# Kernel optimization log

Measured on AMD Instinct MI355X. Metric: run time of the kernel, lower is better.

The kernel has to match this reference:

```python
import jax, jax.numpy as jnp
import numpy as np

EPS = 1e-5  # pyg LayerNorm default eps


def _graph_ln(x):
    # pyg.nn.norm.LayerNorm(affine=False), default mode='graph', batch=None:
    # normalizes over ALL elements of the tensor (x - x.mean()) / x.std(unbiased=False)
    m = x.mean()
    v = jnp.mean((x - m) ** 2)
    return (x - m) * jax.lax.rsqrt(v + EPS)


def _cheb_conv(x, row, col, w, W, b):
    # ChebConv, normalization='sym', lambda_max=2 => scaled Laplacian
    # L_hat = L - I = -D^{-1/2} A D^{-1/2} (self-loops removed, weighted)
    # x: [B,N,C_in], row/col: [E], w: [E], W: [K,C_in,C_out], b: [C_out]
    N = x.shape[1]
    w = jnp.where(row == col, 0.0, w)  # remove_self_loops
    deg = jnp.zeros((N,), x.dtype).at[row].add(w)
    dinv = jnp.where(deg > 0, jax.lax.rsqrt(jnp.maximum(deg, 1e-12)), 0.0)
    norm = -(dinv[row] * w * dinv[col])  # [E]

    def prop(t):  # out[i] += norm_e * t[j] for edge (j=row -> i=col)
        msg = norm[None, :, None] * t[:, row, :]  # [B,E,C]
        return jnp.zeros_like(t).at[:, col, :].add(msg)

    Tx0 = x
    out = jnp.einsum('bnc,cd->bnd', Tx0, W[0])
    Tx1 = prop(x)
    out = out + jnp.einsum('bnc,cd->bnd', Tx1, W[1])
    for k in range(2, W.shape[0]):
        Tx2 = 2.0 * prop(Tx1) - Tx0
        out = out + jnp.einsum('bnc,cd->bnd', Tx2, W[k])
        Tx0, Tx1 = Tx1, Tx2
    return out + b


def setup_inputs() -> dict:
    key = jax.random.key(0)
    ks = jax.random.split(key, 8)
    B, N, C, E, L, K = 8, 2048, 256, 32768, 3, 3
    node_feature = jax.random.normal(ks[0], (B, N, C), dtype=jnp.float32)
    edge_index = jax.random.randint(ks[1], (L, 2, E), 0, N)
    edge_weight = jax.random.uniform(ks[2], (L, E), dtype=jnp.float32)
    s = 1.0 / np.sqrt(C)
    cheb_w = jax.random.normal(ks[3], (L, K, C, C), dtype=jnp.float32) * s
    cheb_b = jnp.zeros((L, C), dtype=jnp.float32)
    mlp_w = jax.random.normal(ks[4], (L, C, C), dtype=jnp.float32) * s
    mlp_b = jax.random.normal(ks[5], (L, C), dtype=jnp.float32) * 0.01
    return {"node_feature": node_feature, "edge_weight": edge_weight,
            "cheb_w": cheb_w, "cheb_b": cheb_b, "mlp_w": mlp_w,
            "mlp_b": mlp_b, "edge_index": edge_index}


def reference(node_feature, edge_weight, cheb_w, cheb_b, mlp_w, mlp_b, edge_index):
    h = node_feature  # [B,N,C]
    L = cheb_w.shape[0]
    for l in range(L):
        h_res = h
        hn = _graph_ln(h)
        hc = _cheb_conv(hn, edge_index[l, 0], edge_index[l, 1],
                        edge_weight[l], cheb_w[l], cheb_b[l])
        h = hc + h_res
        h_res = h
        hn = _graph_ln(h)
        hm = jax.nn.gelu(jnp.einsum('bnc,cd->bnd', hn, mlp_w[l]) + mlp_b[l],
                         approximate=False)  # dropout is identity at inference
        h = hm + h_res
    return h.mean(axis=1)  # [B,C]
```

## Files before the change

kernel.cpp:

```cpp
#include <hip/hip_runtime.h>

#define BATCH   8
#define NNODE   2048
#define CH      256
#define NEDGE   32768
#define NLAYER  3
#define MROWS   (NNODE*BATCH)
#define KCAT    (3*CH)
#define NTOT    (MROWS*CH)

typedef _Float16 half8 __attribute__((ext_vector_type(8)));
typedef _Float16 half4 __attribute__((ext_vector_type(4)));
typedef float    f32x4 __attribute__((ext_vector_type(4)));

#define OFF_ACAT   ((size_t)0)
#define OFF_HF     ((size_t)25165824)
#define OFF_WT     ((size_t)33554432)
#define OFF_MT     ((size_t)34734080)
#define OFF_PARTA  ((size_t)35127296)
#define OFF_PARTB  ((size_t)35135488)
#define OFF_CS     ((size_t)35143680)
#define OFF_CSM    ((size_t)35152896)
#define OFF_DEG    ((size_t)35155968)
#define OFF_CNT    ((size_t)35180544)
#define OFF_ELIST  ((size_t)35205120)
#define OFF_R1     ((size_t)36777984)
#define OFF_R2     ((size_t)36802560)

#define NPART 512

__device__ __forceinline__ void async_lds16(const void* g, void* l) {
  __builtin_amdgcn_global_load_lds((const __attribute__((address_space(1))) void*)g,
                                   (__attribute__((address_space(3))) void*)l, 16, 0, 0);
}

__global__ __launch_bounds__(256) void k_init(const float* __restrict__ x,
                                              _Float16* __restrict__ Acat,
                                              float2* __restrict__ part,
                                              const float* __restrict__ cheb_w,
                                              const float* __restrict__ mlp_w,
                                              _Float16* __restrict__ Wt,
                                              _Float16* __restrict__ Mt,
                                              float* __restrict__ deg,
                                              unsigned int* __restrict__ count) {
  __shared__ float rs[512];
  __shared__ _Float16 lt[64][72];
  const int blk = blockIdx.x, t = threadIdx.x;
  if (blk < 512) {
    int tid = blk*256 + t;
    float s = 0.f, s2 = 0.f;
    for (int i = tid; i < NTOT/4; i += 512*256) {
      int c4 = i & 63, b = (i >> 6) & 7, n = i >> 9;
      float4 v = ((const float4*)x)[((b*NNODE + n) << 6) + c4];
      half4 o; o[0]=(_Float16)v.x; o[1]=(_Float16)v.y; o[2]=(_Float16)v.z; o[3]=(_Float16)v.w;
      *(half4*)&Acat[(size_t)(i >> 6)*KCAT + c4*4] = o;
      s  += v.x + v.y + v.z + v.w;
      s2 += v.x*v.x + v.y*v.y + v.z*v.z + v.w*v.w;
    }
    rs[t] = s; rs[256+t] = s2; __syncthreads();
    for (int o = 128; o > 0; o >>= 1) {
      if (t < o) { rs[t] += rs[t+o]; rs[256+t] += rs[256+t+o]; }
      __syncthreads();
    }
    if (t == 0) part[blk] = make_float2(rs[0], rs[256]);
  } else if (blk < 536) {
    int i = (blk - 512)*256 + t;
    if (i < NLAYER*NNODE) { deg[i] = 0.f; count[i] = 0u; }
  } else {
    const int tile = blk - 536;
    const int rr = t >> 4, c4 = t & 15;
    if (tile < 144) {
      const int l = tile / 48, rem = tile % 48;
      const int kk = rem / 16, q = rem % 16, ci = q >> 2, ni = q & 3;
      const float4* W  = (const float4*)cheb_w + ((size_t)((l*3 + kk)*CH + ci*64))*64 + ni*16;
      const float4* W2 = (const float4*)cheb_w + ((size_t)((l*3 + 2 )*CH + ci*64))*64 + ni*16;
      #pragma unroll
      for (int p = 0; p < 4; ++p) {
        const int r = p*16 + rr;
        float4 v = W[(size_t)r*64 + c4];
        if (kk == 0) {
          float4 v2 = W2[(size_t)r*64 + c4];
          v.x -= v2.x; v.y -= v2.y; v.z -= v2.z; v.w -= v2.w;
        } else if (kk == 2) {
          v.x *= 2.f; v.y *= 2.f; v.z *= 2.f; v.w *= 2.f;
        }
        lt[c4*4+0][r] = (_Float16)v.x; lt[c4*4+1][r] = (_Float16)v.y;
        lt[c4*4+2][r] = (_Float16)v.z; lt[c4*4+3][r] = (_Float16)v.w;
      }
      __syncthreads();
      const int nr = t >> 2, ch2 = t & 3;
      #pragma unroll
      for (int pp = 0; pp < 2; ++pp) {
        const int ch = ch2 + pp*4;
        half8 v = *(const half8*)&lt[nr][ch*8];
        *(half8*)&Wt[((size_t)(l*CH + ni*64 + nr))*KCAT + kk*256 + ci*64 + ch*8] = v;
      }
    } else {
      const int m = tile - 144;
      const int l = m / 16, q = m % 16, ci = q >> 2, ni = q & 3;
      const float4* W = (const float4*)mlp_w + ((size_t)(l*CH + ci*64))*64 + ni*16;
      #pragma unroll
      for (int p = 0; p < 4; ++p) {
        const int r = p*16 + rr;
        float4 v = W[(size_t)r*64 + c4];
        lt[c4*4+0][r] = (_Float16)v.x; lt[c4*4+1][r] = (_Float16)v.y;
        lt[c4*4+2][r] = (_Float16)v.z; lt[c4*4+3][r] = (_Float16)v.w;
      }
      __syncthreads();
      const int nr = t >> 2, ch2 = t & 3;
      #pragma unroll
      for (int pp = 0; pp < 2; ++pp) {
        const int ch = ch2 + pp*4;
        half8 v = *(const half8*)&lt[nr][ch*8];
        *(half8*)&Mt[((size_t)(l*CH + ni*64 + nr))*CH + ci*64 + ch*8] = v;
      }
    }
  }
}

__global__ __launch_bounds__(256) void k_edge_scatter(const int* __restrict__ ei,
                                                      const float* __restrict__ ew,
                                                      float* deg, unsigned int* count,
                                                      unsigned int* elist,
                                                      const _Float16* __restrict__ Wt,
                                                      const _Float16* __restrict__ Mt,
                                                      float* __restrict__ cs,
                                                      float* __restrict__ csM,
                                                      float* __restrict__ out_zero) {
  const int blk = blockIdx.x, t = threadIdx.x;
  if (blk < 384) {
    int i = blk*256 + t;
    int l = i / NEDGE, e = i % NEDGE;
    const int* rows = ei + l*2*NEDGE;
    const int* cols = rows + NEDGE;
    int r = rows[e], c = cols[e];
    float w = (r == c) ? 0.f : ew[i];
    atomicAdd(&deg[l*NNODE + r], w);
    unsigned int slot = atomicAdd(&count[l*NNODE + c], 1u);
    if (slot < 64u) elist[(size_t)(l*NNODE + c)*64 + slot] = (unsigned int)e;
  } else if (blk < 393) {
    int idx = blk - 384, l = idx / 3, kk = idx % 3, n = t;
    const half8* row = (const half8*)&Wt[((size_t)(l*CH + n))*KCAT + kk*256];
    float s = 0.f;
    #pragma unroll 4
    for (int j = 0; j < 32; ++j) {
      half8 v = row[j];
      s += (float)v[0]+(float)v[1]+(float)v[2]+(float)v[3]
         + (float)v[4]+(float)v[5]+(float)v[6]+(float)v[7];
    }
    cs[(l*3 + kk)*CH + n] = s;
  } else if (blk < 396) {
    int l = blk - 393, n = t;
    const half8* row = (const half8*)&Mt[((size_t)(l*CH + n))*CH];
    float s = 0.f;
    #pragma unroll 4
    for (int j = 0; j < 32; ++j) {
      half8 v = row[j];
      s += (float)v[0]+(float)v[1]+(float)v[2]+(float)v[3]
         + (float)v[4]+(float)v[5]+(float)v[6]+(float)v[7];
    }
    csM[l*CH + n] = s;
  } else {
    for (int i = t; i < BATCH*CH; i += 256) out_zero[i] = 0.f;
  }
}

template<int SRC_OFF, int DST_OFF, int RMODE>
__global__ __launch_bounds__(256) void k_prop(_Float16* __restrict__ Acat,
                                              const int* __restrict__ rows,
                                              const float* __restrict__ ew_l,
                                              const float* __restrict__ deg_l,
                                              const unsigned int* __restrict__ count,
                                              const unsigned int* __restrict__ el,
                                              float* __restrict__ r1_l,
                                              float* __restrict__ r2_l) {
  const int blk = blockIdx.x, t = threadIdx.x;
  const int bp = blk & 3, dgrp = blk >> 2;
  const int w = t >> 6, lane = t & 63;
  const int dst = dgrp*4 + w;
  const int b = bp*2 + (lane >> 5), l32 = lane & 31;
  unsigned int c = count[dst]; if (c > 64u) c = 64u;
  const float dc = deg_l[dst];
  const float ic = dc > 0.f ? rsqrtf(fmaxf(dc, 1e-12f)) : 0.f;
  int srcv = 0; float nmv = 0.f;
  if (lane < (int)c) {
    unsigned int e = el[(size_t)dst*64 + lane];
    srcv = rows[e];
    float wv = (srcv == dst) ? 0.f : ew_l[e];
    float dr = deg_l[srcv];
    float ir = dr > 0.f ? rsqrtf(fmaxf(dr, 1e-12f)) : 0.f;
    nmv = -(ir * wv * ic);
  }
  if (RMODE && bp == 0) {
    float rv = nmv;
    if (RMODE == 2) rv = (lane < (int)c) ? nmv * r1_l[srcv] : 0.f;
    #pragma unroll
    for (int o = 32; o > 0; o >>= 1) rv += __shfl_xor(rv, o);
    if (lane == 0) { if (RMODE == 1) r1_l[dst] = rv; else r2_l[dst] = rv; }
  }
  float a0=0.f,a1=0.f,a2=0.f,a3=0.f,a4=0.f,a5=0.f,a6=0.f,a7=0.f;
  const _Float16* base = Acat + SRC_OFF + (size_t)b*KCAT + l32*8;
  #define PROP_STEP(i)                                                            \
    {                                                                             \
      int   src = __builtin_amdgcn_readlane(srcv, (i));                           \
      int   nbi = __builtin_amdgcn_readlane(__builtin_bit_cast(int, nmv), (i));   \
      float nm  = __builtin_bit_cast(float, nbi);                                 \
      half8 v = *(const half8*)&base[(size_t)src*8*KCAT];                         \
      a0 += nm*(float)v[0]; a1 += nm*(float)v[1];                                 \
      a2 += nm*(float)v[2]; a3 += nm*(float)v[3];                                 \
      a4 += nm*(float)v[4]; a5 += nm*(float)v[5];                                 \
      a6 += nm*(float)v[6]; a7 += nm*(float)v[7];                                 \
    }
  unsigned int i = 0;
  for (; i + 4 <= c; i += 4) { PROP_STEP(i) PROP_STEP(i+1) PROP_STEP(i+2) PROP_STEP(i+3) }
  for (; i < c; ++i) { PROP_STEP(i) }
  #undef PROP_STEP
  half8 o;
  o[0]=(_Float16)a0; o[1]=(_Float16)a1; o[2]=(_Float16)a2; o[3]=(_Float16)a3;
  o[4]=(_Float16)a4; o[5]=(_Float16)a5; o[6]=(_Float16)a6; o[7]=(_Float16)a7;
  *(half8*)&Acat[(size_t)(dst*8 + b)*KCAT + DST_OFF + l32*8] = o;
}

template<int KSTEPS, int DO_GELU>
__global__ __launch_bounds__(256) void k_gemm(const _Float16* __restrict__ A, int lda,
                                              const _Float16* __restrict__ Bt, int ldb,
                                              const float* __restrict__ bias,
                                              const float* __restrict__ cs,
                                              const float* __restrict__ r1,
                                              const float* __restrict__ r2,
                                              const float2* __restrict__ part_in,
                                              float2* __restrict__ part_out,
                                              const _Float16* __restrict__ R, int ldr,
                                              _Float16* __restrict__ O, int ldo) {
  __shared__ _Float16 Als[128*64];
  __shared__ _Float16 Bls[64*64];
  __shared__ float red[512];
  __shared__ float mv[2];
  const int bm = blockIdx.x, bn = blockIdx.y;
  const int t = threadIdx.x;
  const int w = t >> 6, lane = t & 63;
  const int quad = lane >> 4, l16 = lane & 15;
  const int rw = w & 1, cw = w >> 1;

  {
    float s = 0.f, s2 = 0.f;
    for (int i = t; i < NPART; i += 256) { float2 p = part_in[i]; s += p.x; s2 += p.y; }
    red[t] = s; red[256+t] = s2; __syncthreads();
    for (int o = 128; o > 0; o >>= 1) {
      if (t < o) { red[t] += red[t+o]; red[256+t] += red[256+t+o]; }
      __syncthreads();
    }
    if (t == 0) {
      float mean = red[0] * (1.f/(float)NTOT);
      float var  = red[256] * (1.f/(float)NTOT) - mean*mean;
      mv[0] = mean; mv[1] = rsqrtf(var + 1e-5f);
    }
    __syncthreads();
  }
  const float mean = mv[0], istd = mv[1];

  f32x4 acc[4][2];
  #pragma unroll
  for (int i = 0; i < 4; ++i)
    #pragma unroll
    for (int j = 0; j < 2; ++j) acc[i][j] = (f32x4){0.f,0.f,0.f,0.f};

  const int cA0 = t, cA1 = 256+t, cA2 = 512+t, cA3 = 768+t;
  const int rA0 = cA0>>3, sA0 = (cA0&7)^(rA0&7);
  const int rA1 = cA1>>3, sA1 = (cA1&7)^(rA1&7);
  const int rA2 = cA2>>3, sA2 = (cA2&7)^(rA2&7);
  const int rA3 = cA3>>3, sA3 = (cA3&7)^(rA3&7);
  const _Float16* ga0 = A + (size_t)(bm*128 + rA0)*lda + sA0*8;
  const _Float16* ga1 = A + (size_t)(bm*128 + rA1)*lda + sA1*8;
  const _Float16* ga2 = A + (size_t)(bm*128 + rA2)*lda + sA2*8;
  const _Float16* ga3 = A + (size_t)(bm*128 + rA3)*lda + sA3*8;
  const _Float16* gb0 = Bt + (size_t)(bn*64 + rA0)*ldb + sA0*8;
  const _Float16* gb1 = Bt + (size_t)(bn*64 + rA1)*ldb + sA1*8;
  _Float16* lA0 = &Als[w*512];
  _Float16* lA1 = &Als[2048 + w*512];
  _Float16* lA2 = &Als[4096 + w*512];
  _Float16* lA3 = &Als[6144 + w*512];
  _Float16* lB0 = &Bls[w*512];
  _Float16* lB1 = &Bls[2048 + w*512];

  for (int ks = 0; ks < KSTEPS; ++ks) {
    async_lds16(ga0, lA0); async_lds16(ga1, lA1);
    async_lds16(ga2, lA2); async_lds16(ga3, lA3);
    async_lds16(gb0, lB0); async_lds16(gb1, lB1);
    ga0 += 64; ga1 += 64; ga2 += 64; ga3 += 64; gb0 += 64; gb1 += 64;
    __syncthreads();
    #pragma unroll
    for (int kh = 0; kh < 2; ++kh) {
      const int q = kh*4 + quad;
      half8 bf[2];
      #pragma unroll
      for (int j = 0; j < 2; ++j) {
        const int rb = cw*32 + j*16 + l16;
        bf[j] = *(const half8*)&Bls[rb*64 + (q ^ (rb & 7))*8];
      }
      #pragma unroll
      for (int i = 0; i < 4; ++i) {
        const int ra = rw*64 + i*16 + l16;
        half8 af = *(const half8*)&Als[ra*64 + (q ^ (ra & 7))*8];
        acc[i][0] = __builtin_amdgcn_mfma_f32_16x16x32_f16(af, bf[0], acc[i][0], 0, 0, 0);
        acc[i][1] = __builtin_amdgcn_mfma_f32_16x16x32_f16(af, bf[1], acc[i][1], 0, 0, 0);
      }
    }
    __syncthreads();
  }

  float s = 0.f, s2 = 0.f;
  const int gm0 = bm*128 + rw*64, gn0 = bn*64 + cw*32;
  const float mi = -mean * istd;
  #pragma unroll
  for (int i = 0; i < 4; ++i) {
    #pragma unroll
    for (int j = 0; j < 2; ++j) {
      f32x4 a = acc[i][j];
      const int col = gn0 + j*16 + l16;
      const float bv = bias[col];
      const float c0v = cs[col];
      float c1v = 0.f, c2v = 0.f;
      if (!DO_GELU) { c1v = cs[256 + col]; c2v = cs[512 + col]; }
      #pragma unroll
      for (int r = 0; r < 4; ++r) {
        const int row = gm0 + i*16 + quad*4 + r;
        float v;
        if (DO_GELU) {
          v = istd*a[r] + mi*c0v + bv;
          v = 0.5f*v*(1.f + erff(v*0.70710678118654752f));
        } else {
          const int node = row >> 3;
          v = istd*a[r] + mi*(c0v + r1[node]*c1v + r2[node]*c2v) + bv;
        }
        float hv = (float)R[(size_t)row*ldr + col] + v;
        O[(size_t)row*ldo + col] = (_Float16)hv;
        s += hv; s2 += hv*hv;
      }
    }
  }
  red[t] = s; red[256+t] = s2; __syncthreads();
  for (int o = 128; o > 0; o >>= 1) {
    if (t < o) { red[t] += red[t+o]; red[256+t] += red[256+t+o]; }
    __syncthreads();
  }
  if (t == 0) part_out[blockIdx.y*gridDim.x + blockIdx.x] = make_float2(red[0], red[256]);
}

__global__ __launch_bounds__(256) void k_mean(const _Float16* __restrict__ Acat,
                                              float* __restrict__ out) {
  int b = blockIdx.x & 7, chunk = blockIdx.x >> 3;
  int c = threadIdx.x;
  float s = 0.f;
  for (int k = 0; k < 256; ++k) {
    int n = chunk*256 + k;
    s += (float)Acat[(size_t)(n*8 + b)*KCAT + c];
  }
  atomicAdd(&out[(b << 8) + c], s * (1.f/(float)NNODE));
}

extern "C" void kernel_launch(void* const* d_in, const int* in_sizes, int n_in,
                              void* d_out, int out_size, void* d_ws, size_t ws_size,
                              hipStream_t stream) {
  const float* x      = (const float*)d_in[0];
  const float* ew     = (const float*)d_in[1];
  const float* cheb_w = (const float*)d_in[2];
  const float* cheb_b = (const float*)d_in[3];
  const float* mlp_w  = (const float*)d_in[4];
  const float* mlp_b  = (const float*)d_in[5];
  const int*   ei     = (const int*)d_in[6];
  float* out = (float*)d_out;

  char* ws = (char*)d_ws;
  _Float16*     Acat  = (_Float16*)(ws + OFF_ACAT);
  _Float16*     Hf    = (_Float16*)(ws + OFF_HF);
  _Float16*     Wt    = (_Float16*)(ws + OFF_WT);
  _Float16*     Mt    = (_Float16*)(ws + OFF_MT);
  float2*       partA = (float2*)(ws + OFF_PARTA);
  float2*       partB = (float2*)(ws + OFF_PARTB);
  float*        cs    = (float*)(ws + OFF_CS);
  float*        csM   = (float*)(ws + OFF_CSM);
  float*        deg   = (float*)(ws + OFF_DEG);
  unsigned int* cnt   = (unsigned int*)(ws + OFF_CNT);
  unsigned int* elist = (unsigned int*)(ws + OFF_ELIST);
  float*        r1    = (float*)(ws + OFF_R1);
  float*        r2    = (float*)(ws + OFF_R2);

  k_init<<<728, 256, 0, stream>>>(x, Acat, partA, cheb_w, mlp_w, Wt, Mt, deg, cnt);
  k_edge_scatter<<<397, 256, 0, stream>>>(ei, ew, deg, cnt, elist, Wt, Mt, cs, csM, out);

  for (int l = 0; l < NLAYER; ++l) {
    const int* rows_l = ei + l*2*NEDGE;
    const float* ew_l = ew + l*NEDGE;
    const float* deg_l = deg + l*NNODE;
    const unsigned int* cnt_l = cnt + l*NNODE;
    const unsigned int* el_l  = elist + (size_t)l*NNODE*64;
    float* r1_l = r1 + l*NNODE;
    float* r2_l = r2 + l*NNODE;

    k_prop<0, 256, 1><<<2048, 256, 0, stream>>>(
        Acat, rows_l, ew_l, deg_l, cnt_l, el_l, r1_l, r2_l);
    k_prop<256, 512, 2><<<2048, 256, 0, stream>>>(
        Acat, rows_l, ew_l, deg_l, cnt_l, el_l, r1_l, r2_l);
    k_gemm<12, 0><<<dim3(128, 4), 256, 0, stream>>>(
        Acat, KCAT, Wt + (size_t)l*CH*KCAT, KCAT, cheb_b + l*CH,
        cs + l*3*CH, r1_l, r2_l, partA, partB,
        Acat, KCAT, Hf, CH);
    k_gemm<4, 1><<<dim3(128, 4), 256, 0, stream>>>(
        Hf, CH, Mt + (size_t)l*CH*CH, CH, mlp_b + l*CH,
        csM + l*CH, r1_l, r2_l, partB, partA,
        Hf, CH, Acat, KCAT);
  }

  k_mean<<<64, 256, 0, stream>>>(Acat, out);
}
```

Measured before the change: 274.8 us.

## Merge edge scatter into init kernel with LDS atomics; double GEMM K-tile

The separate edge-scatter kernel is folded into k_init. Each block now owns a 256-node slice of one layer, scans all edges and accumulates degree and in-edge counts with LDS atomics instead of global atomics. The column sums are computed directly from the fp32 weights, so they no longer depend on Wt/Mt being written first. The GEMM K-step tile is doubled from 64 to 128 with a 16-way XOR swizzle, which halves the number of barrier iterations but doubles shared memory per block and may lower occupancy. The redundant edge scans (each of 24 blocks reads every edge of its layer) add global read traffic, and the order of edge slots can differ from before.

```diff
diff --git a/kernel.cpp b/kernel.cpp
--- a/kernel.cpp
+++ b/kernel.cpp
@@ -39,14 +39,20 @@
                                               float2* __restrict__ part,
                                               const float* __restrict__ cheb_w,
                                               const float* __restrict__ mlp_w,
+                                              const float* __restrict__ ew,
+                                              const int* __restrict__ ei,
                                               _Float16* __restrict__ Wt,
                                               _Float16* __restrict__ Mt,
                                               float* __restrict__ deg,
-                                              unsigned int* __restrict__ count) {
-  __shared__ float rs[512];
-  __shared__ _Float16 lt[64][72];
+                                              unsigned int* __restrict__ cnt,
+                                              unsigned int* __restrict__ elist,
+                                              float* __restrict__ cs,
+                                              float* __restrict__ csM,
+                                              float* __restrict__ out_zero) {
+  __shared__ __align__(16) char smem[9216];
   const int blk = blockIdx.x, t = threadIdx.x;
   if (blk < 512) {
+    float* rs = (float*)smem;
     int tid = blk*256 + t;
     float s = 0.f, s2 = 0.f;
     for (int i = tid; i < NTOT/4; i += 512*256) {
@@ -64,9 +70,29 @@
     }
     if (t == 0) part[blk] = make_float2(rs[0], rs[256]);
   } else if (blk < 536) {
-    int i = (blk - 512)*256 + t;
-    if (i < NLAYER*NNODE) { deg[i] = 0.f; count[i] = 0u; }
-  } else {
+    unsigned int* cnt_lds = (unsigned int*)smem;
+    float*        deg_lds = (float*)(smem + 1024);
+    const int rel = blk - 512, l = rel >> 3, base = (rel & 7) << 8;
+    cnt_lds[t] = 0u; deg_lds[t] = 0.f; __syncthreads();
+    const int* rows = ei + l*2*NEDGE;
+    const int* cols = rows + NEDGE;
+    const float* ewl = ew + l*NEDGE;
+    for (int e = t; e < NEDGE; e += 256) {
+      int r = rows[e], c = cols[e];
+      float wv = (r == c) ? 0.f : ewl[e];
+      int cr = c - base;
+      if ((unsigned)cr < 256u) {
+        unsigned int slot = atomicAdd(&cnt_lds[cr], 1u);
+        if (slot < 64u) elist[((size_t)(l*NNODE + c) << 6) + slot] = (unsigned int)e;
+      }
+      int rr = r - base;
+      if ((unsigned)rr < 256u) atomicAdd(&deg_lds[rr], wv);
+    }
+    __syncthreads();
+    cnt[l*NNODE + base + t] = cnt_lds[t];
+    deg[l*NNODE + base + t] = deg_lds[t];
+  } else if (blk < 728) {
+    _Float16 (*lt)[72] = (_Float16(*)[72])smem;
     const int tile = blk - 536;
     const int rr = t >> 4, c4 = t & 15;
     if (tile < 144) {
@@ -115,51 +141,27 @@
         *(half8*)&Mt[((size_t)(l*CH + ni*64 + nr))*CH + ci*64 + ch*8] = v;
       }
     }
-  }
-}
-
-__global__ __launch_bounds__(256) void k_edge_scatter(const int* __restrict__ ei,
-                                                      const float* __restrict__ ew,
-                                                      float* deg, unsigned int* count,
-                                                      unsigned int* elist,
-                                                      const _Float16* __restrict__ Wt,
-                                                      const _Float16* __restrict__ Mt,
-                                                      float* __restrict__ cs,
-                                                      float* __restrict__ csM,
-                                                      float* __restrict__ out_zero) {
-  const int blk = blockIdx.x, t = threadIdx.x;
-  if (blk < 384) {
-    int i = blk*256 + t;
-    int l = i / NEDGE, e = i % NEDGE;
-    const int* rows = ei + l*2*NEDGE;
-    const int* cols = rows + NEDGE;
-    int r = rows[e], c = cols[e];
-    float w = (r == c) ? 0.f : ew[i];
-    atomicAdd(&deg[l*NNODE + r], w);
-    unsigned int slot = atomicAdd(&count[l*NNODE + c], 1u);
-    if (slot < 64u) elist[(size_t)(l*NNODE + c)*64 + slot] = (unsigned int)e;
-  } else if (blk < 393) {
-    int idx = blk - 384, l = idx / 3, kk = idx % 3, n = t;
-    const half8* row = (const half8*)&Wt[((size_t)(l*CH + n))*KCAT + kk*256];
-    float s = 0.f;
-    #pragma unroll 4
-    for (int j = 0; j < 32; ++j) {
-      half8 v = row[j];
-      s += (float)v[0]+(float)v[1]+(float)v[2]+(float)v[3]
-         + (float)v[4]+(float)v[5]+(float)v[6]+(float)v[7];
-    }
-    cs[(l*3 + kk)*CH + n] = s;
-  } else if (blk < 396) {
-    int l = blk - 393, n = t;
-    const half8* row = (const half8*)&Mt[((size_t)(l*CH + n))*CH];
-    float s = 0.f;
-    #pragma unroll 4
-    for (int j = 0; j < 32; ++j) {
-      half8 v = row[j];
-      s += (float)v[0]+(float)v[1]+(float)v[2]+(float)v[3]
-         + (float)v[4]+(float)v[5]+(float)v[6]+(float)v[7];
-    }
-    csM[l*CH + n] = s;
+  } else if (blk < 740) {
+    const int idx = blk - 728, n = t;
+    if (idx < 9) {
+      const int l = idx / 3, kk = idx % 3;
+      const float* W0 = cheb_w + (size_t)((l*3 + kk)*CH)*CH + n;
+      const float* W2 = cheb_w + (size_t)((l*3 + 2 )*CH)*CH + n;
+      float s = 0.f;
+      for (int cin = 0; cin < CH; ++cin) {
+        float wv = W0[(size_t)cin*CH];
+        if (kk == 0)      wv -= W2[(size_t)cin*CH];
+        else if (kk == 2) wv *= 2.f;
+        s += wv;
+      }
+      cs[(l*3 + kk)*CH + n] = s;
+    } else {
+      const int l = idx - 9;
+      const float* W = mlp_w + (size_t)l*CH*CH + n;
+      float s = 0.f;
+      for (int k2 = 0; k2 < CH; ++k2) s += W[(size_t)k2*CH];
+      csM[l*CH + n] = s;
+    }
   } else {
     for (int i = t; i < BATCH*CH; i += 256) out_zero[i] = 0.f;
   }
@@ -232,8 +234,8 @@
                                               float2* __restrict__ part_out,
                                               const _Float16* __restrict__ R, int ldr,
                                               _Float16* __restrict__ O, int ldo) {
-  __shared__ _Float16 Als[128*64];
-  __shared__ _Float16 Bls[64*64];
+  __shared__ _Float16 Als[128*128];
+  __shared__ _Float16 Bls[64*128];
   __shared__ float red[512];
   __shared__ float mv[2];
   const int bm = blockIdx.x, bn = blockIdx.y;
@@ -265,43 +267,42 @@
     #pragma unroll
     for (int j = 0; j < 2; ++j) acc[i][j] = (f32x4){0.f,0.f,0.f,0.f};
 
-  const int cA0 = t, cA1 = 256+t, cA2 = 512+t, cA3 = 768+t;
-  const int rA0 = cA0>>3, sA0 = (cA0&7)^(rA0&7);
-  const int rA1 = cA1>>3, sA1 = (cA1&7)^(rA1&7);
-  const int rA2 = cA2>>3, sA2 = (cA2&7)^(rA2&7);
-  const int rA3 = cA3>>3, sA3 = (cA3&7)^(rA3&7);
-  const _Float16* ga0 = A + (size_t)(bm*128 + rA0)*lda + sA0*8;
-  const _Float16* ga1 = A + (size_t)(bm*128 + rA1)*lda + sA1*8;
-  const _Float16* ga2 = A + (size_t)(bm*128 + rA2)*lda + sA2*8;
-  const _Float16* ga3 = A + (size_t)(bm*128 + rA3)*lda + sA3*8;
-  const _Float16* gb0 = Bt + (size_t)(bn*64 + rA0)*ldb + sA0*8;
-  const _Float16* gb1 = Bt + (size_t)(bn*64 + rA1)*ldb + sA1*8;
-  _Float16* lA0 = &Als[w*512];
-  _Float16* lA1 = &Als[2048 + w*512];
-  _Float16* lA2 = &Als[4096 + w*512];
-  _Float16* lA3 = &Als[6144 + w*512];
-  _Float16* lB0 = &Bls[w*512];
-  _Float16* lB1 = &Bls[2048 + w*512];
+  const _Float16* ga[8];
+  const _Float16* gb[4];
+  #pragma unroll
+  for (int j = 0; j < 8; ++j) {
+    const int c = j*256 + t, r = c >> 4, s = (c & 15) ^ (r & 15);
+    ga[j] = A + (size_t)(bm*128 + r)*lda + s*8;
+  }
+  #pragma unroll
+  for (int j = 0; j < 4; ++j) {
+    const int c = j*256 + t, r = c >> 4, s = (c & 15) ^ (r & 15);
+    gb[j] = Bt + (size_t)(bn*64 + r)*ldb + s*8;
+  }
 
   for (int ks = 0; ks < KSTEPS; ++ks) {
-    async_lds16(ga0, lA0); async_lds16(ga1, lA1);
-    async_lds16(ga2, lA2); async_lds16(ga3, lA3);
-    async_lds16(gb0, lB0); async_lds16(gb1, lB1);
-    ga0 += 64; ga1 += 64; ga2 += 64; ga3 += 64; gb0 += 64; gb1 += 64;
+    #pragma unroll
+    for (int j = 0; j < 8; ++j) async_lds16(ga[j], &Als[j*2048 + w*512]);
+    #pragma unroll
+    for (int j = 0; j < 4; ++j) async_lds16(gb[j], &Bls[j*2048 + w*512]);
+    #pragma unroll
+    for (int j = 0; j < 8; ++j) ga[j] += 128;
+    #pragma unroll
+    for (int j = 0; j < 4; ++j) gb[j] += 128;
     __syncthreads();
     #pragma unroll
-    for (int kh = 0; kh < 2; ++kh) {
+    for (int kh = 0; kh < 4; ++kh) {
       const int q = kh*4 + quad;
       half8 bf[2];
       #pragma unroll
       for (int j = 0; j < 2; ++j) {
         const int rb = cw*32 + j*16 + l16;
-        bf[j] = *(const half8*)&Bls[rb*64 + (q ^ (rb & 7))*8];
+        bf[j] = *(const half8*)&Bls[rb*128 + (q ^ (rb & 15))*8];
       }
       #pragma unroll
       for (int i = 0; i < 4; ++i) {
         const int ra = rw*64 + i*16 + l16;
-        half8 af = *(const half8*)&Als[ra*64 + (q ^ (ra & 7))*8];
+        half8 af = *(const half8*)&Als[ra*128 + (q ^ (ra & 15))*8];
         acc[i][0] = __builtin_amdgcn_mfma_f32_16x16x32_f16(af, bf[0], acc[i][0], 0, 0, 0);
         acc[i][1] = __builtin_amdgcn_mfma_f32_16x16x32_f16(af, bf[1], acc[i][1], 0, 0, 0);
       }
@@ -386,8 +387,8 @@
   float*        r1    = (float*)(ws + OFF_R1);
   float*        r2    = (float*)(ws + OFF_R2);
 
-  k_init<<<728, 256, 0, stream>>>(x, Acat, partA, cheb_w, mlp_w, Wt, Mt, deg, cnt);
-  k_edge_scatter<<<397, 256, 0, stream>>>(ei, ew, deg, cnt, elist, Wt, Mt, cs, csM, out);
+  k_init<<<741, 256, 0, stream>>>(x, Acat, partA, cheb_w, mlp_w, ew, ei,
+                                  Wt, Mt, deg, cnt, elist, cs, csM, out);
 
   for (int l = 0; l < NLAYER; ++l) {
     const int* rows_l = ei + l*2*NEDGE;
@@ -402,11 +403,11 @@
         Acat, rows_l, ew_l, deg_l, cnt_l, el_l, r1_l, r2_l);
     k_prop<256, 512, 2><<<2048, 256, 0, stream>>>(
         Acat, rows_l, ew_l, deg_l, cnt_l, el_l, r1_l, r2_l);
-    k_gemm<12, 0><<<dim3(128, 4), 256, 0, stream>>>(
+    k_gemm<6, 0><<<dim3(128, 4), 256, 0, stream>>>(
         Acat, KCAT, Wt + (size_t)l*CH*KCAT, KCAT, cheb_b + l*CH,
         cs + l*3*CH, r1_l, r2_l, partA, partB,
         Acat, KCAT, Hf, CH);
-    k_gemm<4, 1><<<dim3(128, 4), 256, 0, stream>>>(
+    k_gemm<2, 1><<<dim3(128, 4), 256, 0, stream>>>(
         Hf, CH, Mt + (size_t)l*CH*CH, CH, mlp_b + l*CH,
         csM + l*CH, r1_l, r2_l, partB, partA,
         Hf, CH, Acat, KCAT);
```

Result: slower. 333.1 us (+21.2%).
